# Kernel optimization log

Hardware: AMD Instinct MI355X
Metric: run time of the kernel (lower is better)

Reference implementation:

```python
import jax, jax.numpy as jnp
import numpy as np

N_EMBED = 64
HEAD_SIZE = 64
B, T = 4096, 128

def setup_inputs() -> dict:
    key = jax.random.key(0)
    k0, k1, k2, k3 = jax.random.split(key, 4)
    x = jax.random.normal(k0, (B, T, N_EMBED), dtype=jnp.float32)
    # nn.Linear(N_EMBED, head_size, bias=False): weight shape [head_size, N_EMBED], y = x @ W.T
    Wq = jax.random.normal(k1, (HEAD_SIZE, N_EMBED), dtype=jnp.float32) * (1.0 / np.sqrt(N_EMBED))
    Wk = jax.random.normal(k2, (HEAD_SIZE, N_EMBED), dtype=jnp.float32) * (1.0 / np.sqrt(N_EMBED))
    Wv = jax.random.normal(k3, (HEAD_SIZE, N_EMBED), dtype=jnp.float32) * (1.0 / np.sqrt(N_EMBED))
    return {"x": x, "Wq": Wq, "Wk": Wk, "Wv": Wv}

def reference(x, Wq, Wk, Wv):
    # q,k,v: [B,T,H]
    q = jnp.einsum('btc,hc->bth', x, Wq)
    k = jnp.einsum('btc,hc->bth', x, Wk)
    v = jnp.einsum('btc,hc->bth', x, Wv)
    scale = HEAD_SIZE ** -0.5
    scores = jnp.einsum('bth,bsh->bts', q, k) * scale  # [B,T,T]
    Tdim = x.shape[1]
    causal = jnp.tril(jnp.ones((Tdim, Tdim), dtype=bool))
    scores = jnp.where(causal, scores, -jnp.inf)
    weights = jax.nn.softmax(scores, axis=-1)
    # dropout disabled (eval mode) for deterministic reference
    out = jnp.einsum('bts,bsh->bth', weights, v)  # [B,T,H]
    return out
```

## Files before the change

### kernel.cpp

```cpp
#include <hip/hip_runtime.h>
#include <hip/hip_bf16.h>

typedef float f4  __attribute__((ext_vector_type(4)));
typedef short s8v __attribute__((ext_vector_type(8)));
typedef short s4v __attribute__((ext_vector_type(4)));

#define MFMA16(a, b, c) __builtin_amdgcn_mfma_f32_16x16x32_bf16((a), (b), (c), 0, 0, 0)

__device__ __forceinline__ unsigned cvtpk(float a, float b) {
  __hip_bfloat162 h2 = __float22bfloat162_rn(make_float2(a, b));
  unsigned u;
  __builtin_memcpy(&u, &h2, 4);
  return u;
}
__device__ __forceinline__ float bf2f(unsigned short s) {
  union { unsigned u; float f; } x; x.u = ((unsigned)s) << 16; return x.f;
}
__device__ __forceinline__ s8v cvt8(const float* p) {
  float4 a = *(const float4*)p;
  float4 b = *(const float4*)(p + 4);
  union { unsigned u[4]; s8v v; } r;
  r.u[0] = cvtpk(a.x, a.y); r.u[1] = cvtpk(a.z, a.w);
  r.u[2] = cvtpk(b.x, b.y); r.u[3] = cvtpk(b.z, b.w);
  return r.v;
}
__device__ __forceinline__ s8v mk8(unsigned a0, unsigned a1, unsigned b0, unsigned b1) {
  union { unsigned u[4]; s8v v; } r;
  r.u[0] = a0; r.u[1] = a1; r.u[2] = b0; r.u[3] = b1;
  return r.v;
}
__device__ __forceinline__ s8v ld44(const short* p0, const short* p1) {
  s4v a = *(const s4v*)p0;
  s4v b = *(const s4v*)p1;
  s8v r;
  r[0] = a[0]; r[1] = a[1]; r[2] = a[2]; r[3] = a[3];
  r[4] = b[0]; r[5] = b[1]; r[6] = b[2]; r[7] = b[3];
  return r;
}

__global__ __launch_bounds__(256, 4)
void attn_head(const void* __restrict__ xg, const void* __restrict__ wqg,
               const void* __restrict__ wkg, const void* __restrict__ wvg,
               void* __restrict__ outg) {
  __shared__ __align__(16) short smem[16384];
  short* Ksm = smem;
  short* Vt  = smem + 8192;

  const int tid  = threadIdx.x;
  const int wave = tid >> 6;
  const int lane = tid & 63;
  const int c16  = lane & 15;
  const int quad = lane >> 4;
  const int b    = blockIdx.x;
  const int swz  = c16 << 2;

  int isbf;
  {
    const unsigned short* w = (const unsigned short*)wqg;
    float f = bf2f(w[lane]);
    float a = fabsf(f);
    int ok = (f == 0.0f || (a >= 1e-4f && a <= 1e4f)) ? 1 : 0;
    unsigned long long ball = __ballot(ok);
    isbf = (__popcll(ball) >= 58) ? 1 : 0;
  }

  const int mts[2] = {wave, 7 - wave};

  s8v xf[2][2];
  #pragma unroll
  for (int mi = 0; mi < 2; mi++) {
    const size_t base = (size_t)b * (128 * 64) + (size_t)(mts[mi] * 16 + c16) * 64;
    #pragma unroll
    for (int kt = 0; kt < 2; kt++) {
      const int off = kt * 32 + quad * 8;
      if (isbf) xf[mi][kt] = *(const s8v*)((const unsigned short*)xg + base + off);
      else      xf[mi][kt] = cvt8((const float*)xg + base + off);
    }
  }

  unsigned qpk[2][4][2];
  #pragma unroll
  for (int ht = 0; ht < 4; ht++) {
    s8v wqf[2], wkf[2], wvf[2];
    const int woff0 = (ht * 16 + c16) * 64 + quad * 8;
    #pragma unroll
    for (int kt = 0; kt < 2; kt++) {
      const int off = woff0 + kt * 32;
      if (isbf) {
        wqf[kt] = *(const s8v*)((const unsigned short*)wqg + off);
        wkf[kt] = *(const s8v*)((const unsigned short*)wkg + off);
        wvf[kt] = *(const s8v*)((const unsigned short*)wvg + off);
      } else {
        wqf[kt] = cvt8((const float*)wqg + off);
        wkf[kt] = cvt8((const float*)wkg + off);
        wvf[kt] = cvt8((const float*)wvg + off);
      }
    }
    #pragma unroll
    for (int mi = 0; mi < 2; mi++) {
      const int m = mts[mi];
      f4 z = {0.f, 0.f, 0.f, 0.f};
      f4 qt = z, kk = z, vv = z;
      qt = MFMA16(wqf[0], xf[mi][0], qt);  qt = MFMA16(wqf[1], xf[mi][1], qt);
      kk = MFMA16(wkf[0], xf[mi][0], kk);  kk = MFMA16(wkf[1], xf[mi][1], kk);
      vv = MFMA16(xf[mi][0], wvf[0], vv);  vv = MFMA16(xf[mi][1], wvf[1], vv);
      qpk[mi][ht][0] = cvtpk(qt[0] * 0.125f, qt[1] * 0.125f);
      qpk[mi][ht][1] = cvtpk(qt[2] * 0.125f, qt[3] * 0.125f);
      {
        union { unsigned u[2]; s4v v; } pk;
        pk.u[0] = cvtpk(kk[0], kk[1]); pk.u[1] = cvtpk(kk[2], kk[3]);
        *(s4v*)(Ksm + (m * 16 + c16) * 64 + ((ht * 16 + quad * 4) ^ swz)) = pk.v;
      }
      {
        union { unsigned u[2]; s4v v; } pv;
        pv.u[0] = cvtpk(vv[0], vv[1]); pv.u[1] = cvtpk(vv[2], vv[3]);
        *(s4v*)(Vt + (ht * 16 + c16) * 128 + ((m * 16 + quad * 4) ^ swz)) = pv.v;
      }
    }
  }

  __syncthreads();

  #pragma unroll
  for (int mi = 0; mi < 2; mi++) {
    const int m = mts[mi];
    const int q4 = quad * 4;
    const s8v qb0 = mk8(qpk[mi][0][0], qpk[mi][0][1], qpk[mi][1][0], qpk[mi][1][1]);
    const s8v qb1 = mk8(qpk[mi][2][0], qpk[mi][2][1], qpk[mi][3][0], qpk[mi][3][1]);

    f4 acc[4];
    #pragma unroll
    for (int ht = 0; ht < 4; ht++) { f4 z = {0.f,0.f,0.f,0.f}; acc[ht] = z; }
    float sum = 0.f;
    const int nchunk = (m >> 1) + 1;

    #pragma unroll
    for (int kt = 0; kt < 4; kt++) {
      if (kt >= nchunk) continue;
      const int nt0 = 2 * kt, nt1 = 2 * kt + 1;
      const bool hb = nt1 <= m;

      f4 z = {0.f, 0.f, 0.f, 0.f};
      f4 s0 = z, s1 = z;
      {
        const short* kr = Ksm + (nt0 * 16 + c16) * 64;
        s0 = MFMA16(ld44(kr + ((q4     ) ^ swz), kr + ((q4 + 16) ^ swz)), qb0, s0);
        s0 = MFMA16(ld44(kr + ((q4 + 32) ^ swz), kr + ((q4 + 48) ^ swz)), qb1, s0);
      }
      if (hb) {
        const short* kr = Ksm + (nt1 * 16 + c16) * 64;
        s1 = MFMA16(ld44(kr + ((q4     ) ^ swz), kr + ((q4 + 16) ^ swz)), qb0, s1);
        s1 = MFMA16(ld44(kr + ((q4 + 32) ^ swz), kr + ((q4 + 48) ^ swz)), qb1, s1);
      }
      #pragma unroll
      for (int r = 0; r < 4; r++) {
        const bool k0 = (nt0 < m) || (q4 + r <= c16);
        float e0 = k0 ? __expf(s0[r]) : 0.0f;
        s0[r] = e0; sum += e0;
      }
      if (hb) {
        #pragma unroll
        for (int r = 0; r < 4; r++) {
          const bool k1 = (nt1 < m) || (q4 + r <= c16);
          float e1 = k1 ? __expf(s1[r]) : 0.0f;
          s1[r] = e1; sum += e1;
        }
      }
      const s8v pb = mk8(cvtpk(s0[0], s0[1]), cvtpk(s0[2], s0[3]),
                         cvtpk(s1[0], s1[1]), cvtpk(s1[2], s1[3]));
      #pragma unroll
      for (int ht = 0; ht < 4; ht++) {
        const short* vr = Vt + (ht * 16 + c16) * 128;
        const s8v va = ld44(vr + ((kt * 32 + q4     ) ^ swz),
                            vr + ((kt * 32 + q4 + 16) ^ swz));
        acc[ht] = MFMA16(va, pb, acc[ht]);
      }
    }

    sum += __shfl_xor(sum, 16);
    sum += __shfl_xor(sum, 32);
    const float inv = 1.0f / sum;

    if (isbf) {
      unsigned short* op = (unsigned short*)outg + (size_t)b * (128 * 64);
      #pragma unroll
      for (int ht = 0; ht < 4; ht++) {
        union { unsigned u[2]; s4v v; } o;
        o.u[0] = cvtpk(acc[ht][0] * inv, acc[ht][1] * inv);
        o.u[1] = cvtpk(acc[ht][2] * inv, acc[ht][3] * inv);
        *(s4v*)(op + (size_t)(m * 16 + c16) * 64 + ht * 16 + q4) = o.v;
      }
    } else {
      float* op = (float*)outg + (size_t)b * (128 * 64);
      #pragma unroll
      for (int ht = 0; ht < 4; ht++) {
        float4 o = {acc[ht][0] * inv, acc[ht][1] * inv,
                    acc[ht][2] * inv, acc[ht][3] * inv};
        *(float4*)(op + (size_t)(m * 16 + c16) * 64 + ht * 16 + q4) = o;
      }
    }
  }
}

extern "C" void kernel_launch(void* const* d_in, const int* in_sizes, int n_in,
                              void* d_out, int out_size, void* d_ws, size_t ws_size,
                              hipStream_t stream) {
  (void)d_ws; (void)ws_size; (void)in_sizes; (void)n_in; (void)out_size;
  attn_head<<<dim3(4096), dim3(256), 0, stream>>>(
      d_in[0], d_in[1], d_in[2], d_in[3], d_out);
}
```

Baseline: 299.8 us.

## Make blocks persistent over four batches and prefetch next batch input

The grid shrinks to 1024 blocks, and each block loops over four batch elements strided by the grid size, reusing its shared memory. For bf16 inputs, the next batch's x fragments are loaded right after the barrier so the load overlaps the attention compute. For fp32 inputs, they are loaded at the end of the iteration after an extra barrier. This aims to cut block scheduling overhead and hide global-load latency, at the cost of an extra sync per iteration and reliance on one resident wave of blocks.

```diff
diff --git a/kernel.cpp b/kernel.cpp
--- a/kernel.cpp
+++ b/kernel.cpp
@@ -38,6 +38,9 @@
   return r;
 }
 
+#define NBLK 1024
+#define NIT  4
+
 __global__ __launch_bounds__(256, 4)
 void attn_head(const void* __restrict__ xg, const void* __restrict__ wqg,
                const void* __restrict__ wkg, const void* __restrict__ wvg,
@@ -51,7 +54,7 @@
   const int lane = tid & 63;
   const int c16  = lane & 15;
   const int quad = lane >> 4;
-  const int b    = blockIdx.x;
+  const int b0   = blockIdx.x;
   const int swz  = c16 << 2;
 
   int isbf;
@@ -65,138 +68,168 @@
   }
 
   const int mts[2] = {wave, 7 - wave};
+  int xoff[2][2];
+  #pragma unroll
+  for (int mi = 0; mi < 2; mi++)
+    #pragma unroll
+    for (int kt = 0; kt < 2; kt++)
+      xoff[mi][kt] = (mts[mi] * 16 + c16) * 64 + kt * 32 + quad * 8;
 
   s8v xf[2][2];
   #pragma unroll
-  for (int mi = 0; mi < 2; mi++) {
-    const size_t base = (size_t)b * (128 * 64) + (size_t)(mts[mi] * 16 + c16) * 64;
+  for (int mi = 0; mi < 2; mi++)
     #pragma unroll
     for (int kt = 0; kt < 2; kt++) {
-      const int off = kt * 32 + quad * 8;
-      if (isbf) xf[mi][kt] = *(const s8v*)((const unsigned short*)xg + base + off);
-      else      xf[mi][kt] = cvt8((const float*)xg + base + off);
-    }
-  }
-
-  unsigned qpk[2][4][2];
-  #pragma unroll
-  for (int ht = 0; ht < 4; ht++) {
-    s8v wqf[2], wkf[2], wvf[2];
-    const int woff0 = (ht * 16 + c16) * 64 + quad * 8;
-    #pragma unroll
-    for (int kt = 0; kt < 2; kt++) {
-      const int off = woff0 + kt * 32;
-      if (isbf) {
-        wqf[kt] = *(const s8v*)((const unsigned short*)wqg + off);
-        wkf[kt] = *(const s8v*)((const unsigned short*)wkg + off);
-        wvf[kt] = *(const s8v*)((const unsigned short*)wvg + off);
-      } else {
-        wqf[kt] = cvt8((const float*)wqg + off);
-        wkf[kt] = cvt8((const float*)wkg + off);
-        wvf[kt] = cvt8((const float*)wvg + off);
-      }
-    }
+      if (isbf) xf[mi][kt] = *(const s8v*)((const unsigned short*)xg +
+                                           (size_t)b0 * 8192 + xoff[mi][kt]);
+      else      xf[mi][kt] = cvt8((const float*)xg + (size_t)b0 * 8192 + xoff[mi][kt]);
+    }
+
+  for (int it = 0; it < NIT; ++it) {
+    const int b = b0 + NBLK * it;
+
+    unsigned qpk[2][4][2];
+    #pragma unroll
+    for (int ht = 0; ht < 4; ht++) {
+      s8v wqf[2], wkf[2], wvf[2];
+      const int woff0 = (ht * 16 + c16) * 64 + quad * 8;
+      #pragma unroll
+      for (int kt = 0; kt < 2; kt++) {
+        const int off = woff0 + kt * 32;
+        if (isbf) {
+          wqf[kt] = *(const s8v*)((const unsigned short*)wqg + off);
+          wkf[kt] = *(const s8v*)((const unsigned short*)wkg + off);
+          wvf[kt] = *(const s8v*)((const unsigned short*)wvg + off);
+        } else {
+          wqf[kt] = cvt8((const float*)wqg + off);
+          wkf[kt] = cvt8((const float*)wkg + off);
+          wvf[kt] = cvt8((const float*)wvg + off);
+        }
+      }
+      #pragma unroll
+      for (int mi = 0; mi < 2; mi++) {
+        const int m = mts[mi];
+        f4 z = {0.f, 0.f, 0.f, 0.f};
+        f4 qt = z, kk = z, vv = z;
+        qt = MFMA16(wqf[0], xf[mi][0], qt);  qt = MFMA16(wqf[1], xf[mi][1], qt);
+        kk = MFMA16(wkf[0], xf[mi][0], kk);  kk = MFMA16(wkf[1], xf[mi][1], kk);
+        vv = MFMA16(xf[mi][0], wvf[0], vv);  vv = MFMA16(xf[mi][1], wvf[1], vv);
+        qpk[mi][ht][0] = cvtpk(qt[0] * 0.125f, qt[1] * 0.125f);
+        qpk[mi][ht][1] = cvtpk(qt[2] * 0.125f, qt[3] * 0.125f);
+        {
+          union { unsigned u[2]; s4v v; } pk;
+          pk.u[0] = cvtpk(kk[0], kk[1]); pk.u[1] = cvtpk(kk[2], kk[3]);
+          *(s4v*)(Ksm + (m * 16 + c16) * 64 + ((ht * 16 + quad * 4) ^ swz)) = pk.v;
+        }
+        {
+          union { unsigned u[2]; s4v v; } pv;
+          pv.u[0] = cvtpk(vv[0], vv[1]); pv.u[1] = cvtpk(vv[2], vv[3]);
+          *(s4v*)(Vt + (ht * 16 + c16) * 128 + ((m * 16 + quad * 4) ^ swz)) = pv.v;
+        }
+      }
+    }
+
+    __syncthreads();
+
+    if (isbf && it + 1 < NIT) {
+      const unsigned short* xb = (const unsigned short*)xg +
+                                 (size_t)(b + NBLK) * 8192;
+      #pragma unroll
+      for (int mi = 0; mi < 2; mi++)
+        #pragma unroll
+        for (int kt = 0; kt < 2; kt++)
+          xf[mi][kt] = *(const s8v*)(xb + xoff[mi][kt]);
+    }
+
     #pragma unroll
     for (int mi = 0; mi < 2; mi++) {
       const int m = mts[mi];
-      f4 z = {0.f, 0.f, 0.f, 0.f};
-      f4 qt = z, kk = z, vv = z;
-      qt = MFMA16(wqf[0], xf[mi][0], qt);  qt = MFMA16(wqf[1], xf[mi][1], qt);
-      kk = MFMA16(wkf[0], xf[mi][0], kk);  kk = MFMA16(wkf[1], xf[mi][1], kk);
-      vv = MFMA16(xf[mi][0], wvf[0], vv);  vv = MFMA16(xf[mi][1], wvf[1], vv);
-      qpk[mi][ht][0] = cvtpk(qt[0] * 0.125f, qt[1] * 0.125f);
-      qpk[mi][ht][1] = cvtpk(qt[2] * 0.125f, qt[3] * 0.125f);
-      {
-        union { unsigned u[2]; s4v v; } pk;
-        pk.u[0] = cvtpk(kk[0], kk[1]); pk.u[1] = cvtpk(kk[2], kk[3]);
-        *(s4v*)(Ksm + (m * 16 + c16) * 64 + ((ht * 16 + quad * 4) ^ swz)) = pk.v;
-      }
-      {
-        union { unsigned u[2]; s4v v; } pv;
-        pv.u[0] = cvtpk(vv[0], vv[1]); pv.u[1] = cvtpk(vv[2], vv[3]);
-        *(s4v*)(Vt + (ht * 16 + c16) * 128 + ((m * 16 + quad * 4) ^ swz)) = pv.v;
-      }
-    }
-  }
-
-  __syncthreads();
-
-  #pragma unroll
-  for (int mi = 0; mi < 2; mi++) {
-    const int m = mts[mi];
-    const int q4 = quad * 4;
-    const s8v qb0 = mk8(qpk[mi][0][0], qpk[mi][0][1], qpk[mi][1][0], qpk[mi][1][1]);
-    const s8v qb1 = mk8(qpk[mi][2][0], qpk[mi][2][1], qpk[mi][3][0], qpk[mi][3][1]);
-
-    f4 acc[4];
-    #pragma unroll
-    for (int ht = 0; ht < 4; ht++) { f4 z = {0.f,0.f,0.f,0.f}; acc[ht] = z; }
-    float sum = 0.f;
-    const int nchunk = (m >> 1) + 1;
-
-    #pragma unroll
-    for (int kt = 0; kt < 4; kt++) {
-      if (kt >= nchunk) continue;
-      const int nt0 = 2 * kt, nt1 = 2 * kt + 1;
-      const bool hb = nt1 <= m;
-
-      f4 z = {0.f, 0.f, 0.f, 0.f};
-      f4 s0 = z, s1 = z;
-      {
-        const short* kr = Ksm + (nt0 * 16 + c16) * 64;
-        s0 = MFMA16(ld44(kr + ((q4     ) ^ swz), kr + ((q4 + 16) ^ swz)), qb0, s0);
-        s0 = MFMA16(ld44(kr + ((q4 + 32) ^ swz), kr + ((q4 + 48) ^ swz)), qb1, s0);
-      }
-      if (hb) {
-        const short* kr = Ksm + (nt1 * 16 + c16) * 64;
-        s1 = MFMA16(ld44(kr + ((q4     ) ^ swz), kr + ((q4 + 16) ^ swz)), qb0, s1);
-        s1 = MFMA16(ld44(kr + ((q4 + 32) ^ swz), kr + ((q4 + 48) ^ swz)), qb1, s1);
-      }
-      #pragma unroll
-      for (int r = 0; r < 4; r++) {
-        const bool k0 = (nt0 < m) || (q4 + r <= c16);
-        float e0 = k0 ? __expf(s0[r]) : 0.0f;
-        s0[r] = e0; sum += e0;
-      }
-      if (hb) {
+      const int q4 = quad * 4;
+      const s8v qb0 = mk8(qpk[mi][0][0], qpk[mi][0][1], qpk[mi][1][0], qpk[mi][1][1]);
+      const s8v qb1 = mk8(qpk[mi][2][0], qpk[mi][2][1], qpk[mi][3][0], qpk[mi][3][1]);
+
+      f4 acc[4];
+      #pragma unroll
+      for (int ht = 0; ht < 4; ht++) { f4 z = {0.f,0.f,0.f,0.f}; acc[ht] = z; }
+      float sum = 0.f;
+      const int nchunk = (m >> 1) + 1;
+
+      #pragma unroll
+      for (int kt = 0; kt < 4; kt++) {
+        if (kt >= nchunk) continue;
+        const int nt0 = 2 * kt, nt1 = 2 * kt + 1;
+        const bool hb = nt1 <= m;
+
+        f4 z = {0.f, 0.f, 0.f, 0.f};
+        f4 s0 = z, s1 = z;
+        {
+          const short* kr = Ksm + (nt0 * 16 + c16) * 64;
+          s0 = MFMA16(ld44(kr + ((q4     ) ^ swz), kr + ((q4 + 16) ^ swz)), qb0, s0);
+          s0 = MFMA16(ld44(kr + ((q4 + 32) ^ swz), kr + ((q4 + 48) ^ swz)), qb1, s0);
+        }
+        if (hb) {
+          const short* kr = Ksm + (nt1 * 16 + c16) * 64;
+          s1 = MFMA16(ld44(kr + ((q4     ) ^ swz), kr + ((q4 + 16) ^ swz)), qb0, s1);
+          s1 = MFMA16(ld44(kr + ((q4 + 32) ^ swz), kr + ((q4 + 48) ^ swz)), qb1, s1);
+        }
         #pragma unroll
         for (int r = 0; r < 4; r++) {
-          const bool k1 = (nt1 < m) || (q4 + r <= c16);
-          float e1 = k1 ? __expf(s1[r]) : 0.0f;
-          s1[r] = e1; sum += e1;
-        }
-      }
-      const s8v pb = mk8(cvtpk(s0[0], s0[1]), cvtpk(s0[2], s0[3]),
-                         cvtpk(s1[0], s1[1]), cvtpk(s1[2], s1[3]));
-      #pragma unroll
-      for (int ht = 0; ht < 4; ht++) {
-        const short* vr = Vt + (ht * 16 + c16) * 128;
-        const s8v va = ld44(vr + ((kt * 32 + q4     ) ^ swz),
-                            vr + ((kt * 32 + q4 + 16) ^ swz));
-        acc[ht] = MFMA16(va, pb, acc[ht]);
-      }
-    }
-
-    sum += __shfl_xor(sum, 16);
-    sum += __shfl_xor(sum, 32);
-    const float inv = 1.0f / sum;
-
-    if (isbf) {
-      unsigned short* op = (unsigned short*)outg + (size_t)b * (128 * 64);
-      #pragma unroll
-      for (int ht = 0; ht < 4; ht++) {
-        union { unsigned u[2]; s4v v; } o;
-        o.u[0] = cvtpk(acc[ht][0] * inv, acc[ht][1] * inv);
-        o.u[1] = cvtpk(acc[ht][2] * inv, acc[ht][3] * inv);
-        *(s4v*)(op + (size_t)(m * 16 + c16) * 64 + ht * 16 + q4) = o.v;
-      }
-    } else {
-      float* op = (float*)outg + (size_t)b * (128 * 64);
-      #pragma unroll
-      for (int ht = 0; ht < 4; ht++) {
-        float4 o = {acc[ht][0] * inv, acc[ht][1] * inv,
-                    acc[ht][2] * inv, acc[ht][3] * inv};
-        *(float4*)(op + (size_t)(m * 16 + c16) * 64 + ht * 16 + q4) = o;
+          const bool k0 = (nt0 < m) || (q4 + r <= c16);
+          float e0 = k0 ? __expf(s0[r]) : 0.0f;
+          s0[r] = e0; sum += e0;
+        }
+        if (hb) {
+          #pragma unroll
+          for (int r = 0; r < 4; r++) {
+            const bool k1 = (nt1 < m) || (q4 + r <= c16);
+            float e1 = k1 ? __expf(s1[r]) : 0.0f;
+            s1[r] = e1; sum += e1;
+          }
+        }
+        const s8v pb = mk8(cvtpk(s0[0], s0[1]), cvtpk(s0[2], s0[3]),
+                           cvtpk(s1[0], s1[1]), cvtpk(s1[2], s1[3]));
+        #pragma unroll
+        for (int ht = 0; ht < 4; ht++) {
+          const short* vr = Vt + (ht * 16 + c16) * 128;
+          const s8v va = ld44(vr + ((kt * 32 + q4     ) ^ swz),
+                              vr + ((kt * 32 + q4 + 16) ^ swz));
+          acc[ht] = MFMA16(va, pb, acc[ht]);
+        }
+      }
+
+      sum += __shfl_xor(sum, 16);
+      sum += __shfl_xor(sum, 32);
+      const float inv = 1.0f / sum;
+
+      if (isbf) {
+        unsigned short* op = (unsigned short*)outg + (size_t)b * 8192;
+        #pragma unroll
+        for (int ht = 0; ht < 4; ht++) {
+          union { unsigned u[2]; s4v v; } o;
+          o.u[0] = cvtpk(acc[ht][0] * inv, acc[ht][1] * inv);
+          o.u[1] = cvtpk(acc[ht][2] * inv, acc[ht][3] * inv);
+          *(s4v*)(op + (size_t)(m * 16 + c16) * 64 + ht * 16 + q4) = o.v;
+        }
+      } else {
+        float* op = (float*)outg + (size_t)b * 8192;
+        #pragma unroll
+        for (int ht = 0; ht < 4; ht++) {
+          float4 o = {acc[ht][0] * inv, acc[ht][1] * inv,
+                      acc[ht][2] * inv, acc[ht][3] * inv};
+          *(float4*)(op + (size_t)(m * 16 + c16) * 64 + ht * 16 + q4) = o;
+        }
+      }
+    }
+
+    if (it + 1 < NIT) {
+      __syncthreads();
+      if (!isbf) {
+        const float* xb = (const float*)xg + (size_t)(b + NBLK) * 8192;
+        #pragma unroll
+        for (int mi = 0; mi < 2; mi++)
+          #pragma unroll
+          for (int kt = 0; kt < 2; kt++)
+            xf[mi][kt] = cvt8(xb + xoff[mi][kt]);
       }
     }
   }
@@ -206,6 +239,6 @@
                               void* d_out, int out_size, void* d_ws, size_t ws_size,
                               hipStream_t stream) {
   (void)d_ws; (void)ws_size; (void)in_sizes; (void)n_in; (void)out_size;
-  attn_head<<<dim3(4096), dim3(256), 0, stream>>>(
+  attn_head<<<dim3(NBLK), dim3(256), 0, stream>>>(
       d_in[0], d_in[1], d_in[2], d_in[3], d_out);
 }
```

Result: slower. 348.5 us (+16.2%).

## Use one wave per query tile with 512-thread blocks

Applied to the files above, without the earlier changes.

The kernel switches from 4 waves each handling two paired query tiles (m and 7-m) to 8 waves each handling a single 16-row query tile, launched with 512 threads per block. This doubles per-block parallelism and cuts per-wave registers, which aims to shorten latency chains and raise occupancy. In exchange, the causal work is now unbalanced across waves (wave 7 does four key chunks, wave 0 does one), and every wave reloads the three weight matrices, adding redundant weight loads.

```diff
diff --git a/kernel.cpp b/kernel.cpp
--- a/kernel.cpp
+++ b/kernel.cpp
@@ -38,7 +38,7 @@
   return r;
 }
 
-__global__ __launch_bounds__(256, 4)
+__global__ __launch_bounds__(512, 4)
 void attn_head(const void* __restrict__ xg, const void* __restrict__ wqg,
                const void* __restrict__ wkg, const void* __restrict__ wvg,
                void* __restrict__ outg) {
@@ -47,12 +47,13 @@
   short* Vt  = smem + 8192;
 
   const int tid  = threadIdx.x;
-  const int wave = tid >> 6;
+  const int m    = tid >> 6;
   const int lane = tid & 63;
   const int c16  = lane & 15;
   const int quad = lane >> 4;
   const int b    = blockIdx.x;
   const int swz  = c16 << 2;
+  const int q4   = quad * 4;
 
   int isbf;
   {
@@ -64,21 +65,18 @@
     isbf = (__popcll(ball) >= 58) ? 1 : 0;
   }
 
-  const int mts[2] = {wave, 7 - wave};
-
-  s8v xf[2][2];
-  #pragma unroll
-  for (int mi = 0; mi < 2; mi++) {
-    const size_t base = (size_t)b * (128 * 64) + (size_t)(mts[mi] * 16 + c16) * 64;
+  s8v xf[2];
+  {
+    const size_t base = (size_t)b * 8192 + (size_t)(m * 16 + c16) * 64;
     #pragma unroll
     for (int kt = 0; kt < 2; kt++) {
       const int off = kt * 32 + quad * 8;
-      if (isbf) xf[mi][kt] = *(const s8v*)((const unsigned short*)xg + base + off);
-      else      xf[mi][kt] = cvt8((const float*)xg + base + off);
-    }
-  }
-
-  unsigned qpk[2][4][2];
+      if (isbf) xf[kt] = *(const s8v*)((const unsigned short*)xg + base + off);
+      else      xf[kt] = cvt8((const float*)xg + base + off);
+    }
+  }
+
+  unsigned qpk[4][2];
   #pragma unroll
   for (int ht = 0; ht < 4; ht++) {
     s8v wqf[2], wkf[2], wvf[2];
@@ -96,108 +94,99 @@
         wvf[kt] = cvt8((const float*)wvg + off);
       }
     }
-    #pragma unroll
-    for (int mi = 0; mi < 2; mi++) {
-      const int m = mts[mi];
-      f4 z = {0.f, 0.f, 0.f, 0.f};
-      f4 qt = z, kk = z, vv = z;
-      qt = MFMA16(wqf[0], xf[mi][0], qt);  qt = MFMA16(wqf[1], xf[mi][1], qt);
-      kk = MFMA16(wkf[0], xf[mi][0], kk);  kk = MFMA16(wkf[1], xf[mi][1], kk);
-      vv = MFMA16(xf[mi][0], wvf[0], vv);  vv = MFMA16(xf[mi][1], wvf[1], vv);
-      qpk[mi][ht][0] = cvtpk(qt[0] * 0.125f, qt[1] * 0.125f);
-      qpk[mi][ht][1] = cvtpk(qt[2] * 0.125f, qt[3] * 0.125f);
-      {
-        union { unsigned u[2]; s4v v; } pk;
-        pk.u[0] = cvtpk(kk[0], kk[1]); pk.u[1] = cvtpk(kk[2], kk[3]);
-        *(s4v*)(Ksm + (m * 16 + c16) * 64 + ((ht * 16 + quad * 4) ^ swz)) = pk.v;
-      }
-      {
-        union { unsigned u[2]; s4v v; } pv;
-        pv.u[0] = cvtpk(vv[0], vv[1]); pv.u[1] = cvtpk(vv[2], vv[3]);
-        *(s4v*)(Vt + (ht * 16 + c16) * 128 + ((m * 16 + quad * 4) ^ swz)) = pv.v;
-      }
+    f4 z = {0.f, 0.f, 0.f, 0.f};
+    f4 qt = z, kk = z, vv = z;
+    qt = MFMA16(wqf[0], xf[0], qt);  qt = MFMA16(wqf[1], xf[1], qt);
+    kk = MFMA16(wkf[0], xf[0], kk);  kk = MFMA16(wkf[1], xf[1], kk);
+    vv = MFMA16(xf[0], wvf[0], vv);  vv = MFMA16(xf[1], wvf[1], vv);
+    qpk[ht][0] = cvtpk(qt[0] * 0.125f, qt[1] * 0.125f);
+    qpk[ht][1] = cvtpk(qt[2] * 0.125f, qt[3] * 0.125f);
+    {
+      union { unsigned u[2]; s4v v; } pk;
+      pk.u[0] = cvtpk(kk[0], kk[1]); pk.u[1] = cvtpk(kk[2], kk[3]);
+      *(s4v*)(Ksm + (m * 16 + c16) * 64 + ((ht * 16 + q4) ^ swz)) = pk.v;
+    }
+    {
+      union { unsigned u[2]; s4v v; } pv;
+      pv.u[0] = cvtpk(vv[0], vv[1]); pv.u[1] = cvtpk(vv[2], vv[3]);
+      *(s4v*)(Vt + (ht * 16 + c16) * 128 + ((m * 16 + q4) ^ swz)) = pv.v;
     }
   }
 
   __syncthreads();
 
+  const s8v qb0 = mk8(qpk[0][0], qpk[0][1], qpk[1][0], qpk[1][1]);
+  const s8v qb1 = mk8(qpk[2][0], qpk[2][1], qpk[3][0], qpk[3][1]);
+
+  f4 acc[4];
   #pragma unroll
-  for (int mi = 0; mi < 2; mi++) {
-    const int m = mts[mi];
-    const int q4 = quad * 4;
-    const s8v qb0 = mk8(qpk[mi][0][0], qpk[mi][0][1], qpk[mi][1][0], qpk[mi][1][1]);
-    const s8v qb1 = mk8(qpk[mi][2][0], qpk[mi][2][1], qpk[mi][3][0], qpk[mi][3][1]);
-
-    f4 acc[4];
-    #pragma unroll
-    for (int ht = 0; ht < 4; ht++) { f4 z = {0.f,0.f,0.f,0.f}; acc[ht] = z; }
-    float sum = 0.f;
-    const int nchunk = (m >> 1) + 1;
-
-    #pragma unroll
-    for (int kt = 0; kt < 4; kt++) {
-      if (kt >= nchunk) continue;
-      const int nt0 = 2 * kt, nt1 = 2 * kt + 1;
-      const bool hb = nt1 <= m;
-
-      f4 z = {0.f, 0.f, 0.f, 0.f};
-      f4 s0 = z, s1 = z;
-      {
-        const short* kr = Ksm + (nt0 * 16 + c16) * 64;
-        s0 = MFMA16(ld44(kr + ((q4     ) ^ swz), kr + ((q4 + 16) ^ swz)), qb0, s0);
-        s0 = MFMA16(ld44(kr + ((q4 + 32) ^ swz), kr + ((q4 + 48) ^ swz)), qb1, s0);
-      }
-      if (hb) {
-        const short* kr = Ksm + (nt1 * 16 + c16) * 64;
-        s1 = MFMA16(ld44(kr + ((q4     ) ^ swz), kr + ((q4 + 16) ^ swz)), qb0, s1);
-        s1 = MFMA16(ld44(kr + ((q4 + 32) ^ swz), kr + ((q4 + 48) ^ swz)), qb1, s1);
-      }
+  for (int ht = 0; ht < 4; ht++) { f4 z = {0.f,0.f,0.f,0.f}; acc[ht] = z; }
+  float sum = 0.f;
+  const int nchunk = (m >> 1) + 1;
+
+  #pragma unroll
+  for (int kt = 0; kt < 4; kt++) {
+    if (kt >= nchunk) continue;
+    const int nt0 = 2 * kt, nt1 = 2 * kt + 1;
+    const bool hb = nt1 <= m;
+
+    f4 z = {0.f, 0.f, 0.f, 0.f};
+    f4 s0 = z, s1 = z;
+    {
+      const short* kr = Ksm + (nt0 * 16 + c16) * 64;
+      s0 = MFMA16(ld44(kr + ((q4     ) ^ swz), kr + ((q4 + 16) ^ swz)), qb0, s0);
+      s0 = MFMA16(ld44(kr + ((q4 + 32) ^ swz), kr + ((q4 + 48) ^ swz)), qb1, s0);
+    }
+    if (hb) {
+      const short* kr = Ksm + (nt1 * 16 + c16) * 64;
+      s1 = MFMA16(ld44(kr + ((q4     ) ^ swz), kr + ((q4 + 16) ^ swz)), qb0, s1);
+      s1 = MFMA16(ld44(kr + ((q4 + 32) ^ swz), kr + ((q4 + 48) ^ swz)), qb1, s1);
+    }
+    #pragma unroll
+    for (int r = 0; r < 4; r++) {
+      const bool k0 = (nt0 < m) || (q4 + r <= c16);
+      float e0 = k0 ? __expf(s0[r]) : 0.0f;
+      s0[r] = e0; sum += e0;
+    }
+    if (hb) {
       #pragma unroll
       for (int r = 0; r < 4; r++) {
-        const bool k0 = (nt0 < m) || (q4 + r <= c16);
-        float e0 = k0 ? __expf(s0[r]) : 0.0f;
-        s0[r] = e0; sum += e0;
+        const bool k1 = (nt1 < m) || (q4 + r <= c16);
+        float e1 = k1 ? __expf(s1[r]) : 0.0f;
+        s1[r] = e1; sum += e1;
       }
-      if (hb) {
-        #pragma unroll
-        for (int r = 0; r < 4; r++) {
-          const bool k1 = (nt1 < m) || (q4 + r <= c16);
-          float e1 = k1 ? __expf(s1[r]) : 0.0f;
-          s1[r] = e1; sum += e1;
-        }
-      }
-      const s8v pb = mk8(cvtpk(s0[0], s0[1]), cvtpk(s0[2], s0[3]),
-                         cvtpk(s1[0], s1[1]), cvtpk(s1[2], s1[3]));
-      #pragma unroll
-      for (int ht = 0; ht < 4; ht++) {
-        const short* vr = Vt + (ht * 16 + c16) * 128;
-        const s8v va = ld44(vr + ((kt * 32 + q4     ) ^ swz),
-                            vr + ((kt * 32 + q4 + 16) ^ swz));
-        acc[ht] = MFMA16(va, pb, acc[ht]);
-      }
-    }
-
-    sum += __shfl_xor(sum, 16);
-    sum += __shfl_xor(sum, 32);
-    const float inv = 1.0f / sum;
-
-    if (isbf) {
-      unsigned short* op = (unsigned short*)outg + (size_t)b * (128 * 64);
-      #pragma unroll
-      for (int ht = 0; ht < 4; ht++) {
-        union { unsigned u[2]; s4v v; } o;
-        o.u[0] = cvtpk(acc[ht][0] * inv, acc[ht][1] * inv);
-        o.u[1] = cvtpk(acc[ht][2] * inv, acc[ht][3] * inv);
-        *(s4v*)(op + (size_t)(m * 16 + c16) * 64 + ht * 16 + q4) = o.v;
-      }
-    } else {
-      float* op = (float*)outg + (size_t)b * (128 * 64);
-      #pragma unroll
-      for (int ht = 0; ht < 4; ht++) {
-        float4 o = {acc[ht][0] * inv, acc[ht][1] * inv,
-                    acc[ht][2] * inv, acc[ht][3] * inv};
-        *(float4*)(op + (size_t)(m * 16 + c16) * 64 + ht * 16 + q4) = o;
-      }
+    }
+    const s8v pb = mk8(cvtpk(s0[0], s0[1]), cvtpk(s0[2], s0[3]),
+                       cvtpk(s1[0], s1[1]), cvtpk(s1[2], s1[3]));
+    #pragma unroll
+    for (int ht = 0; ht < 4; ht++) {
+      const short* vr = Vt + (ht * 16 + c16) * 128;
+      const s8v va = ld44(vr + ((kt * 32 + q4     ) ^ swz),
+                          vr + ((kt * 32 + q4 + 16) ^ swz));
+      acc[ht] = MFMA16(va, pb, acc[ht]);
+    }
+  }
+
+  sum += __shfl_xor(sum, 16);
+  sum += __shfl_xor(sum, 32);
+  const float inv = 1.0f / sum;
+
+  if (isbf) {
+    unsigned short* op = (unsigned short*)outg + (size_t)b * 8192;
+    #pragma unroll
+    for (int ht = 0; ht < 4; ht++) {
+      union { unsigned u[2]; s4v v; } o;
+      o.u[0] = cvtpk(acc[ht][0] * inv, acc[ht][1] * inv);
+      o.u[1] = cvtpk(acc[ht][2] * inv, acc[ht][3] * inv);
+      *(s4v*)(op + (size_t)(m * 16 + c16) * 64 + ht * 16 + q4) = o.v;
+    }
+  } else {
+    float* op = (float*)outg + (size_t)b * 8192;
+    #pragma unroll
+    for (int ht = 0; ht < 4; ht++) {
+      float4 o = {acc[ht][0] * inv, acc[ht][1] * inv,
+                  acc[ht][2] * inv, acc[ht][3] * inv};
+      *(float4*)(op + (size_t)(m * 16 + c16) * 64 + ht * 16 + q4) = o;
     }
   }
 }
@@ -206,6 +195,6 @@
                               void* d_out, int out_size, void* d_ws, size_t ws_size,
                               hipStream_t stream) {
   (void)d_ws; (void)ws_size; (void)in_sizes; (void)n_in; (void)out_size;
-  attn_head<<<dim3(4096), dim3(256), 0, stream>>>(
+  attn_head<<<dim3(4096), dim3(512), 0, stream>>>(
       d_in[0], d_in[1], d_in[2], d_in[3], d_out);
 }
```

After: 368.7 us. +23.0%, slower.
